# Optimization experiments

Hardware: AMD Instinct MI355X
Metric: run time of the kernel (lower is better)

Reference implementation:

```python
import jax, jax.numpy as jnp
import numpy as np

DIM = 1024
HEADS = 16
SCALE = DIM ** -0.5  # NOTE: original uses full dim, not head dim


def setup_inputs() -> dict:
    key = jax.random.key(0)
    k1, k2, k3, k4 = jax.random.split(key, 4)
    x = jax.random.normal(k1, (2, 2048, DIM), dtype=jnp.float32)
    # torch nn.Linear(dim, 3*dim, bias=False): y = x @ W_qkv (stored here as [dim, 3*dim])
    w_qkv = jax.random.normal(k2, (DIM, 3 * DIM), dtype=jnp.float32) * (DIM ** -0.5)
    w_out = jax.random.normal(k3, (DIM, DIM), dtype=jnp.float32) * (DIM ** -0.5)
    b_out = jax.random.normal(k4, (DIM,), dtype=jnp.float32) * 0.01
    return {"x": x, "w_qkv": w_qkv, "w_out": w_out, "b_out": b_out}


def reference(x, w_qkv, w_out, b_out):
    b, n, d = x.shape
    h = HEADS
    hd = d // h
    qkv = x @ w_qkv  # [b, n, 3*d]
    # last dim layout is (qkv, h, hd) per rearrange 'b n (qkv h d) -> qkv b h n d'
    qkv = qkv.reshape(b, n, 3, h, hd)
    q, k, v = (jnp.moveaxis(qkv, (2, 3), (0, 2))[i] for i in range(3))  # each [b, h, n, hd]
    dots = jnp.einsum('bhid,bhjd->bhij', q, k) * SCALE
    causal_mask = jnp.triu(jnp.ones((n, n), dtype=bool), k=1)
    dots = jnp.where(causal_mask, -jnp.inf, dots)
    attn = jax.nn.softmax(dots, axis=-1)
    out = jnp.einsum('bhij,bhjd->bhid', attn, v)
    out = jnp.moveaxis(out, 1, 2).reshape(b, n, d)  # 'b h n d -> b n (h d)'
    return out @ w_out + b_out
```

## Files before the change

### kernel.cpp

```cpp
#include <hip/hip_runtime.h>

typedef __attribute__((ext_vector_type(8))) short bf16x8;
typedef __attribute__((ext_vector_type(4))) float f32x4;
typedef unsigned short u16;
typedef unsigned int u32;

#define SEQ 2048
#define NHEAD 16
#define EXP2_SCALE 0.045084219f

__device__ __forceinline__ u16 f2bf(float f){
  u32 u = __builtin_bit_cast(u32, f);
  u += 0x7FFFu + ((u >> 16) & 1u);
  return (u16)(u >> 16);
}

__device__ __forceinline__ void gl16(const u16* g, u16* l){
  __builtin_amdgcn_global_load_lds(
      (__attribute__((address_space(1))) void*)(unsigned long long)(const void*)g,
      (__attribute__((address_space(3))) void*)(unsigned)(unsigned long long)(const void*)l,
      16, 0, 0);
}

__global__ __launch_bounds__(256) void prep(const float* __restrict__ x,
                                            const float* __restrict__ w_qkv,
                                            const float* __restrict__ w_out,
                                            u16* __restrict__ xb,
                                            u16* __restrict__ wqkvT,
                                            u16* __restrict__ woutT){
  __shared__ u16 t[32][33];
  const int bid = blockIdx.x;
  if (bid < 4096){
    int i = (bid * 256 + threadIdx.x) << 2;
    float4 v = *(const float4*)&x[i];
    ushort4 o;
    o.x = f2bf(v.x); o.y = f2bf(v.y); o.z = f2bf(v.z); o.w = f2bf(v.w);
    *(ushort4*)&xb[i] = o;
    return;
  }
  const float* src; u16* dst; int R, C, bx, by;
  if (bid < 7168){ int tt = bid - 4096; src = w_qkv; dst = wqkvT; R = 1024; C = 3072; bx = tt % 96; by = tt / 96; }
  else           { int tt = bid - 7168; src = w_out; dst = woutT; R = 1024; C = 1024; bx = tt % 32; by = tt / 32; }
  const int c0 = bx << 5, r0 = by << 5;
  const int tx = threadIdx.x & 31, tg = threadIdx.x >> 5;
  #pragma unroll
  for (int i = 0; i < 4; i++){
    int r = (tg << 2) + i;
    t[r][tx] = f2bf(src[(size_t)(r0 + r) * C + (c0 + tx)]);
  }
  __syncthreads();
  #pragma unroll
  for (int i = 0; i < 4; i++){
    int c = (tg << 2) + i;
    dst[(size_t)(c0 + c) * R + (r0 + tx)] = t[tx][c];
  }
}

__global__ __launch_bounds__(256) void gemm_qkv(const u16* __restrict__ A,
                                                const u16* __restrict__ Bt,
                                                u16* __restrict__ Qo,
                                                u16* __restrict__ Ko,
                                                u16* __restrict__ Vto){
  __shared__ u16 As[128 * 64];
  __shared__ u16 Bs[128 * 64];
  const int tid = threadIdx.x;
  const int lane = tid & 63, wid = tid >> 6;
  const int l15 = lane & 15, quad = lane >> 4;
  const int wm = wid >> 1, wn = wid & 1;
  const int bm = blockIdx.y << 7, bn = blockIdx.x << 7;
  const int qkv_idx = bn >> 10;

  const int lr = lane >> 3;
  const int cc = (lane & 7) ^ lr;
  const u16* gA0 = A  + (size_t)(bm + wid * 32 + lr) * 1024 + (cc << 3);
  const u16* gB0 = Bt + (size_t)(bn + wid * 32 + lr) * 1024 + (cc << 3);
  u16* lA0 = &As[wid * 2048];
  u16* lB0 = &Bs[wid * 2048];

  f32x4 acc[4][4];
  #pragma unroll
  for (int i = 0; i < 4; i++)
    #pragma unroll
    for (int j = 0; j < 4; j++) acc[i][j] = (f32x4){0.f, 0.f, 0.f, 0.f};

  const bool vbranch = (qkv_idx == 2);
  for (int k0 = 0; k0 < 1024; k0 += 64){
    #pragma unroll
    for (int t = 0; t < 4; t++){
      gl16(gA0 + k0 + t * 8192, lA0 + t * 512);
      gl16(gB0 + k0 + t * 8192, lB0 + t * 512);
    }
    __syncthreads();
    #pragma unroll
    for (int hf = 0; hf < 2; hf++){
      bf16x8 af[4], bfr[4];
      #pragma unroll
      for (int mt = 0; mt < 4; mt++){
        int row = wm * 64 + mt * 16 + l15;
        af[mt] = *(const bf16x8*)&As[row * 64 + (((hf * 4 + quad) ^ (row & 7)) << 3)];
      }
      #pragma unroll
      for (int nt = 0; nt < 4; nt++){
        int row = wn * 64 + nt * 16 + l15;
        bfr[nt] = *(const bf16x8*)&Bs[row * 64 + (((hf * 4 + quad) ^ (row & 7)) << 3)];
      }
      if (!vbranch){
        #pragma unroll
        for (int mt = 0; mt < 4; mt++)
          #pragma unroll
          for (int nt = 0; nt < 4; nt++)
            acc[mt][nt] = __builtin_amdgcn_mfma_f32_16x16x32_bf16(af[mt], bfr[nt], acc[mt][nt], 0, 0, 0);
      } else {
        #pragma unroll
        for (int mt = 0; mt < 4; mt++)
          #pragma unroll
          for (int nt = 0; nt < 4; nt++)
            acc[mt][nt] = __builtin_amdgcn_mfma_f32_16x16x32_bf16(bfr[nt], af[mt], acc[mt][nt], 0, 0, 0);
      }
    }
    __syncthreads();
  }

  if (!vbranch){
    const float qscale = (qkv_idx == 0) ? EXP2_SCALE : 1.0f;
    #pragma unroll
    for (int mt = 0; mt < 4; mt++){
      #pragma unroll
      for (int nt = 0; nt < 4; nt++){
        int col = bn + wn * 64 + nt * 16 + l15;
        int head = (col & 1023) >> 6, hd_i = col & 63;
        #pragma unroll
        for (int r = 0; r < 4; r++){
          int row = bm + wm * 64 + mt * 16 + quad * 4 + r;
          int b = row >> 11, pos = row & 2047;
          size_t bh = ((size_t)(b * NHEAD + head)) << 17;
          u16 v = f2bf(acc[mt][nt][r] * qscale);
          if (qkv_idx == 0) Qo[bh + ((size_t)pos << 6) + hd_i] = v;
          else              Ko[bh + ((size_t)pos << 6) + hd_i] = v;
        }
      }
    }
  } else {
    #pragma unroll
    for (int mt = 0; mt < 4; mt++){
      int row_m = bm + wm * 64 + mt * 16 + l15;
      int b = row_m >> 11, pos = row_m & 2047;
      #pragma unroll
      for (int nt = 0; nt < 4; nt++){
        #pragma unroll
        for (int r = 0; r < 4; r++){
          int c = bn + wn * 64 + nt * 16 + quad * 4 + r;
          int head = (c & 1023) >> 6, hd_i = c & 63;
          size_t bh = ((size_t)(b * NHEAD + head)) << 17;
          Vto[bh + ((size_t)hd_i << 11) + pos] = f2bf(acc[mt][nt][r]);
        }
      }
    }
  }
}

__global__ __launch_bounds__(256) void attn_kernel(const u16* __restrict__ Q,
                                                   const u16* __restrict__ K,
                                                   const u16* __restrict__ Vt,
                                                   u16* __restrict__ Oo){
  __shared__ u16 Ks[128 * 64];
  __shared__ u16 Vts[64 * 128];
  __shared__ u16 Ps[4][16 * 136];
  const int tid = threadIdx.x;
  const int lane = tid & 63, wid = tid >> 6;
  const int l15 = lane & 15, quad = lane >> 4;
  const int bh = blockIdx.x & 31;
  const int qt = 31 - (blockIdx.x >> 5);
  const size_t base = ((size_t)bh) << 17;
  const int b = bh >> 4, h = bh & 15;

  const u16* qsrc = Q + base + ((size_t)((qt << 6) + wid * 16 + l15) << 6) + quad * 8;
  const bf16x8 bq0 = *(const bf16x8*)qsrc;
  const bf16x8 bq1 = *(const bf16x8*)(qsrc + 32);

  const int rK = wid * 32 + (lane >> 3);
  const int cK = (lane & 7) ^ (rK & 7);
  const u16* gK0 = K + base + ((size_t)rK << 6) + (cK << 3);
  u16* lK = &Ks[wid * 2048];
  const u16* gV[4];
  #pragma unroll
  for (int t = 0; t < 4; t++){
    int rv = wid * 16 + t * 4 + (lane >> 4);
    int cv = (lane & 15) ^ (rv & 15);
    gV[t] = Vt + base + (size_t)rv * 2048 + (cv << 3);
  }
  u16* lV = &Vts[wid * 2048];

  f32x4 o[4];
  #pragma unroll
  for (int dt = 0; dt < 4; dt++) o[dt] = (f32x4){0.f, 0.f, 0.f, 0.f};
  float lsum = 0.f;
  const int qpos = (qt << 6) + wid * 16 + l15;
  const int jt_max = qt >> 1;
  u16* Pw = &Ps[wid][0];

  auto kv_iter = [&](const int jt, const bool diag) __attribute__((always_inline)) {
    const u16* gk = gK0 + (size_t)jt * 8192;
    #pragma unroll
    for (int t = 0; t < 4; t++) gl16(gk + t * 512, lK + t * 512);
    #pragma unroll
    for (int t = 0; t < 4; t++) gl16(gV[t] + (jt << 7), lV + t * 512);
    __syncthreads();

    f32x4 st[8];
    #pragma unroll
    for (int mt = 0; mt < 8; mt++) st[mt] = (f32x4){0.f, 0.f, 0.f, 0.f};
    #pragma unroll
    for (int mt = 0; mt < 8; mt++){
      int kvr = mt * 16 + l15;
      bf16x8 ak0 = *(const bf16x8*)&Ks[kvr * 64 + ((quad ^ (kvr & 7)) << 3)];
      st[mt] = __builtin_amdgcn_mfma_f32_16x16x32_bf16(ak0, bq0, st[mt], 0, 0, 0);
      bf16x8 ak1 = *(const bf16x8*)&Ks[kvr * 64 + (((4 + quad) ^ (kvr & 7)) << 3)];
      st[mt] = __builtin_amdgcn_mfma_f32_16x16x32_bf16(ak1, bq1, st[mt], 0, 0, 0);
    }

    #pragma unroll
    for (int mt = 0; mt < 8; mt++){
      float pr[4];
      #pragma unroll
      for (int r = 0; r < 4; r++){
        float w = st[mt][r];
        if (diag){
          int kv = (jt << 7) + mt * 16 + quad * 4 + r;
          if (kv > qpos) w = -INFINITY;
        }
        pr[r] = __builtin_amdgcn_exp2f(w);
      }
      lsum += (pr[0] + pr[1]) + (pr[2] + pr[3]);
      u32 a0 = __builtin_bit_cast(u32, pr[0]) + 0x8000u;
      u32 a1 = __builtin_bit_cast(u32, pr[1]) + 0x8000u;
      u32 a2 = __builtin_bit_cast(u32, pr[2]) + 0x8000u;
      u32 a3 = __builtin_bit_cast(u32, pr[3]) + 0x8000u;
      uint2 pk;
      pk.x = __builtin_amdgcn_perm(a1, a0, 0x07060302u);
      pk.y = __builtin_amdgcn_perm(a3, a2, 0x07060302u);
      *(uint2*)&Pw[l15 * 136 + mt * 16 + quad * 4] = pk;
    }

    #pragma unroll
    for (int ks = 0; ks < 4; ks++){
      bf16x8 bp = *(const bf16x8*)&Pw[l15 * 136 + ks * 32 + quad * 8];
      #pragma unroll
      for (int dt = 0; dt < 4; dt++){
        int dr = dt * 16 + l15;
        bf16x8 av = *(const bf16x8*)&Vts[dr * 128 + (((ks * 4 + quad) ^ (dr & 15)) << 3)];
        o[dt] = __builtin_amdgcn_mfma_f32_16x16x32_bf16(av, bp, o[dt], 0, 0, 0);
      }
    }
    __syncthreads();
  };

  for (int jt = 0; jt < jt_max; jt++) kv_iter(jt, false);
  kv_iter(jt_max, true);

  lsum += __shfl_xor(lsum, 16);
  lsum += __shfl_xor(lsum, 32);
  float inv = 1.f / lsum;
  const size_t orow = (size_t)((b << 11) + qpos) * 1024 + h * 64;
  #pragma unroll
  for (int dt = 0; dt < 4; dt++){
    ushort4 w;
    w.x = f2bf(o[dt][0] * inv); w.y = f2bf(o[dt][1] * inv);
    w.z = f2bf(o[dt][2] * inv); w.w = f2bf(o[dt][3] * inv);
    *(ushort4*)&Oo[orow + dt * 16 + quad * 4] = w;
  }
}

__global__ __launch_bounds__(256) void gemm_out(const u16* __restrict__ A,
                                                const u16* __restrict__ Bt,
                                                const float* __restrict__ bias,
                                                float* __restrict__ out){
  __shared__ u16 As[128 * 64];
  __shared__ u16 Bs[128 * 64];
  const int tid = threadIdx.x;
  const int lane = tid & 63, wid = tid >> 6;
  const int l15 = lane & 15, quad = lane >> 4;
  const int wm = wid >> 1, wn = wid & 1;
  const int bm = blockIdx.y << 7, bn = blockIdx.x << 7;

  const int lr = lane >> 3;
  const int cc = (lane & 7) ^ lr;
  const u16* gA0 = A  + (size_t)(bm + wid * 32 + lr) * 1024 + (cc << 3);
  const u16* gB0 = Bt + (size_t)(bn + wid * 32 + lr) * 1024 + (cc << 3);
  u16* lA0 = &As[wid * 2048];
  u16* lB0 = &Bs[wid * 2048];

  f32x4 acc[4][4];
  #pragma unroll
  for (int i = 0; i < 4; i++)
    #pragma unroll
    for (int j = 0; j < 4; j++) acc[i][j] = (f32x4){0.f, 0.f, 0.f, 0.f};

  for (int k0 = 0; k0 < 1024; k0 += 64){
    #pragma unroll
    for (int t = 0; t < 4; t++){
      gl16(gA0 + k0 + t * 8192, lA0 + t * 512);
      gl16(gB0 + k0 + t * 8192, lB0 + t * 512);
    }
    __syncthreads();
    #pragma unroll
    for (int hf = 0; hf < 2; hf++){
      bf16x8 af[4], bfr[4];
      #pragma unroll
      for (int mt = 0; mt < 4; mt++){
        int row = wm * 64 + mt * 16 + l15;
        af[mt] = *(const bf16x8*)&As[row * 64 + (((hf * 4 + quad) ^ (row & 7)) << 3)];
      }
      #pragma unroll
      for (int nt = 0; nt < 4; nt++){
        int row = wn * 64 + nt * 16 + l15;
        bfr[nt] = *(const bf16x8*)&Bs[row * 64 + (((hf * 4 + quad) ^ (row & 7)) << 3)];
      }
      #pragma unroll
      for (int mt = 0; mt < 4; mt++)
        #pragma unroll
        for (int nt = 0; nt < 4; nt++)
          acc[mt][nt] = __builtin_amdgcn_mfma_f32_16x16x32_bf16(af[mt], bfr[nt], acc[mt][nt], 0, 0, 0);
    }
    __syncthreads();
  }

  #pragma unroll
  for (int nt = 0; nt < 4; nt++){
    int col = bn + wn * 64 + nt * 16 + l15;
    float bv = bias[col];
    #pragma unroll
    for (int mt = 0; mt < 4; mt++)
      #pragma unroll
      for (int r = 0; r < 4; r++){
        int row = bm + wm * 64 + mt * 16 + quad * 4 + r;
        out[(size_t)row * 1024 + col] = acc[mt][nt][r] + bv;
      }
  }
}

extern "C" void kernel_launch(void* const* d_in, const int* in_sizes, int n_in,
                              void* d_out, int out_size, void* d_ws, size_t ws_size,
                              hipStream_t stream){
  const float* x     = (const float*)d_in[0];
  const float* w_qkv = (const float*)d_in[1];
  const float* w_out = (const float*)d_in[2];
  const float* b_out = (const float*)d_in[3];
  float* out = (float*)d_out;

  char* ws = (char*)d_ws;
  u16* xb    = (u16*)(ws);
  u16* wqkvT = (u16*)(ws + (8u  << 20));
  u16* woutT = (u16*)(ws + (14u << 20));
  u16* Qb    = (u16*)(ws + (16u << 20));
  u16* Kb    = (u16*)(ws + (24u << 20));
  u16* Vtb   = (u16*)(ws + (32u << 20));
  u16* attn  = (u16*)(ws + (40u << 20));

  prep<<<8192, 256, 0, stream>>>(x, w_qkv, w_out, xb, wqkvT, woutT);
  gemm_qkv<<<dim3(24, 32), 256, 0, stream>>>(xb, wqkvT, Qb, Kb, Vtb);
  attn_kernel<<<dim3(1024), 256, 0, stream>>>(Qb, Kb, Vtb, attn);
  gemm_out<<<dim3(8, 32), 256, 0, stream>>>(attn, woutT, b_out, out);
}
```

Baseline: 175.8 us.

## Double attention query tile to 128 rows and vectorize GEMM epilogue stores

```diff
diff --git a/kernel.cpp b/kernel.cpp
--- a/kernel.cpp
+++ b/kernel.cpp
@@ -83,7 +83,6 @@
     #pragma unroll
     for (int j = 0; j < 4; j++) acc[i][j] = (f32x4){0.f, 0.f, 0.f, 0.f};
 
-  const bool vbranch = (qkv_idx == 2);
   for (int k0 = 0; k0 < 1024; k0 += 64){
     #pragma unroll
     for (int t = 0; t < 4; t++){
@@ -104,107 +103,99 @@
         int row = wn * 64 + nt * 16 + l15;
         bfr[nt] = *(const bf16x8*)&Bs[row * 64 + (((hf * 4 + quad) ^ (row & 7)) << 3)];
       }
-      if (!vbranch){
+      #pragma unroll
+      for (int mt = 0; mt < 4; mt++)
         #pragma unroll
-        for (int mt = 0; mt < 4; mt++)
-          #pragma unroll
-          for (int nt = 0; nt < 4; nt++)
-            acc[mt][nt] = __builtin_amdgcn_mfma_f32_16x16x32_bf16(af[mt], bfr[nt], acc[mt][nt], 0, 0, 0);
-      } else {
-        #pragma unroll
-        for (int mt = 0; mt < 4; mt++)
-          #pragma unroll
-          for (int nt = 0; nt < 4; nt++)
-            acc[mt][nt] = __builtin_amdgcn_mfma_f32_16x16x32_bf16(bfr[nt], af[mt], acc[mt][nt], 0, 0, 0);
-      }
-    }
-    __syncthreads();
-  }
-
-  if (!vbranch){
-    const float qscale = (qkv_idx == 0) ? EXP2_SCALE : 1.0f;
+        for (int nt = 0; nt < 4; nt++)
+          acc[mt][nt] = __builtin_amdgcn_mfma_f32_16x16x32_bf16(bfr[nt], af[mt], acc[mt][nt], 0, 0, 0);
+    }
+    __syncthreads();
+  }
+
+  if (qkv_idx != 2){
+    const float qs = (qkv_idx == 0) ? EXP2_SCALE : 1.0f;
+    u16* dst = (qkv_idx == 0) ? Qo : Ko;
     #pragma unroll
     for (int mt = 0; mt < 4; mt++){
+      int xr = bm + wm * 64 + mt * 16 + l15;
+      int b = xr >> 11, pos = xr & 2047;
       #pragma unroll
       for (int nt = 0; nt < 4; nt++){
-        int col = bn + wn * 64 + nt * 16 + l15;
-        int head = (col & 1023) >> 6, hd_i = col & 63;
-        #pragma unroll
-        for (int r = 0; r < 4; r++){
-          int row = bm + wm * 64 + mt * 16 + quad * 4 + r;
-          int b = row >> 11, pos = row & 2047;
-          size_t bh = ((size_t)(b * NHEAD + head)) << 17;
-          u16 v = f2bf(acc[mt][nt][r] * qscale);
-          if (qkv_idx == 0) Qo[bh + ((size_t)pos << 6) + hd_i] = v;
-          else              Ko[bh + ((size_t)pos << 6) + hd_i] = v;
-        }
+        int c0 = bn + wn * 64 + nt * 16 + quad * 4;
+        int head = (c0 & 1023) >> 6, hd0 = c0 & 63;
+        size_t bhh = ((size_t)(b * NHEAD + head)) << 17;
+        ushort4 w;
+        w.x = f2bf(acc[mt][nt][0] * qs); w.y = f2bf(acc[mt][nt][1] * qs);
+        w.z = f2bf(acc[mt][nt][2] * qs); w.w = f2bf(acc[mt][nt][3] * qs);
+        *(ushort4*)&dst[bhh + ((size_t)pos << 6) + hd0] = w;
       }
     }
   } else {
     #pragma unroll
     for (int mt = 0; mt < 4; mt++){
-      int row_m = bm + wm * 64 + mt * 16 + l15;
-      int b = row_m >> 11, pos = row_m & 2047;
+      int xr = bm + wm * 64 + mt * 16 + l15;
+      int b = xr >> 11, pos = xr & 2047;
       #pragma unroll
       for (int nt = 0; nt < 4; nt++){
         #pragma unroll
         for (int r = 0; r < 4; r++){
           int c = bn + wn * 64 + nt * 16 + quad * 4 + r;
           int head = (c & 1023) >> 6, hd_i = c & 63;
-          size_t bh = ((size_t)(b * NHEAD + head)) << 17;
-          Vto[bh + ((size_t)hd_i << 11) + pos] = f2bf(acc[mt][nt][r]);
+          size_t bhh = ((size_t)(b * NHEAD + head)) << 17;
+          Vto[bhh + ((size_t)hd_i << 11) + pos] = f2bf(acc[mt][nt][r]);
         }
       }
     }
   }
 }
 
-__global__ __launch_bounds__(256) void attn_kernel(const u16* __restrict__ Q,
-                                                   const u16* __restrict__ K,
-                                                   const u16* __restrict__ Vt,
-                                                   u16* __restrict__ Oo){
+__global__ __launch_bounds__(512, 4) void attn_kernel(const u16* __restrict__ Q,
+                                                      const u16* __restrict__ K,
+                                                      const u16* __restrict__ Vt,
+                                                      u16* __restrict__ Oo){
   __shared__ u16 Ks[128 * 64];
   __shared__ u16 Vts[64 * 128];
-  __shared__ u16 Ps[4][16 * 136];
+  __shared__ u16 Ps[8][16 * 136];
   const int tid = threadIdx.x;
   const int lane = tid & 63, wid = tid >> 6;
   const int l15 = lane & 15, quad = lane >> 4;
   const int bh = blockIdx.x & 31;
-  const int qt = 31 - (blockIdx.x >> 5);
+  const int j = blockIdx.x >> 5;
+  const int qt2 = (j < 8) ? (15 - j) : (j - 8);
   const size_t base = ((size_t)bh) << 17;
   const int b = bh >> 4, h = bh & 15;
 
-  const u16* qsrc = Q + base + ((size_t)((qt << 6) + wid * 16 + l15) << 6) + quad * 8;
+  const u16* qsrc = Q + base + ((size_t)((qt2 << 7) + wid * 16 + l15) << 6) + quad * 8;
   const bf16x8 bq0 = *(const bf16x8*)qsrc;
   const bf16x8 bq1 = *(const bf16x8*)(qsrc + 32);
 
-  const int rK = wid * 32 + (lane >> 3);
+  const int rK = wid * 16 + (lane >> 3);
   const int cK = (lane & 7) ^ (rK & 7);
   const u16* gK0 = K + base + ((size_t)rK << 6) + (cK << 3);
-  u16* lK = &Ks[wid * 2048];
-  const u16* gV[4];
-  #pragma unroll
-  for (int t = 0; t < 4; t++){
-    int rv = wid * 16 + t * 4 + (lane >> 4);
+  u16* lK = &Ks[wid * 1024];
+  const u16* gV[2];
+  #pragma unroll
+  for (int t = 0; t < 2; t++){
+    int rv = wid * 8 + t * 4 + (lane >> 4);
     int cv = (lane & 15) ^ (rv & 15);
     gV[t] = Vt + base + (size_t)rv * 2048 + (cv << 3);
   }
-  u16* lV = &Vts[wid * 2048];
+  u16* lV = &Vts[wid * 1024];
 
   f32x4 o[4];
   #pragma unroll
   for (int dt = 0; dt < 4; dt++) o[dt] = (f32x4){0.f, 0.f, 0.f, 0.f};
   float lsum = 0.f;
-  const int qpos = (qt << 6) + wid * 16 + l15;
-  const int jt_max = qt >> 1;
+  const int qpos = (qt2 << 7) + wid * 16 + l15;
+  const int jt_max = qt2;
   u16* Pw = &Ps[wid][0];
 
   auto kv_iter = [&](const int jt, const bool diag) __attribute__((always_inline)) {
     const u16* gk = gK0 + (size_t)jt * 8192;
-    #pragma unroll
-    for (int t = 0; t < 4; t++) gl16(gk + t * 512, lK + t * 512);
-    #pragma unroll
-    for (int t = 0; t < 4; t++) gl16(gV[t] + (jt << 7), lV + t * 512);
+    gl16(gk,       lK);
+    gl16(gk + 512, lK + 512);
+    gl16(gV[0] + (jt << 7), lV);
+    gl16(gV[1] + (jt << 7), lV + 512);
     __syncthreads();
 
     f32x4 st[8];
@@ -320,22 +311,23 @@
       for (int mt = 0; mt < 4; mt++)
         #pragma unroll
         for (int nt = 0; nt < 4; nt++)
-          acc[mt][nt] = __builtin_amdgcn_mfma_f32_16x16x32_bf16(af[mt], bfr[nt], acc[mt][nt], 0, 0, 0);
+          acc[mt][nt] = __builtin_amdgcn_mfma_f32_16x16x32_bf16(bfr[nt], af[mt], acc[mt][nt], 0, 0, 0);
     }
     __syncthreads();
   }
 
   #pragma unroll
   for (int nt = 0; nt < 4; nt++){
-    int col = bn + wn * 64 + nt * 16 + l15;
-    float bv = bias[col];
-    #pragma unroll
-    for (int mt = 0; mt < 4; mt++)
-      #pragma unroll
-      for (int r = 0; r < 4; r++){
-        int row = bm + wm * 64 + mt * 16 + quad * 4 + r;
-        out[(size_t)row * 1024 + col] = acc[mt][nt][r] + bv;
-      }
+    int c0 = bn + wn * 64 + nt * 16 + quad * 4;
+    float4 bv = *(const float4*)&bias[c0];
+    #pragma unroll
+    for (int mt = 0; mt < 4; mt++){
+      int row = bm + wm * 64 + mt * 16 + l15;
+      float4 w;
+      w.x = acc[mt][nt][0] + bv.x; w.y = acc[mt][nt][1] + bv.y;
+      w.z = acc[mt][nt][2] + bv.z; w.w = acc[mt][nt][3] + bv.w;
+      *(float4*)&out[(size_t)row * 1024 + c0] = w;
+    }
   }
 }
 
@@ -359,6 +351,6 @@
 
   prep<<<8192, 256, 0, stream>>>(x, w_qkv, w_out, xb, wqkvT, woutT);
   gemm_qkv<<<dim3(24, 32), 256, 0, stream>>>(xb, wqkvT, Qb, Kb, Vtb);
-  attn_kernel<<<dim3(1024), 256, 0, stream>>>(Qb, Kb, Vtb, attn);
+  attn_kernel<<<dim3(512), 512, 0, stream>>>(Qb, Kb, Vtb, attn);
   gemm_out<<<dim3(8, 32), 256, 0, stream>>>(attn, woutT, b_out, out);
 }
```

After: 177.9 us. No clear change (+1.2%).
